# Kernel tuning notes

Hardware: AMD Instinct MI355X
Metric: run time of the kernel (lower is better)

Reference implementation:

```python
import jax, jax.numpy as jnp
import numpy as np
from jax import lax


def _conv_layer(x, K, k, stride, pad):
    """Faithful reimplementation of the custom Conv2d, including its two quirks:
    1) weight/input flatten-order mismatch: K.reshape(k*k*cin, cout) pairs flat
       index m (decoded as kh,kw,cin for K) against x flattened as (cin,kh,kw),
       so the effective conv weight is K.reshape(-1,cout).reshape(cin,k,k,cout).
    2) the python loop range(0, padd-k, stride) misses the last valid position
       whenever (padd-k) is divisible by stride, leaving last row/col zero.
    """
    B, cin, s_in, _ = x.shape
    cout = K.shape[-1]
    out_size = (s_in + 2 * pad - k) // stride + 1
    padd = s_in + 2 * pad
    n_loop = -(-(padd - k) // stride)  # = len(range(0, padd-k, stride))
    xp = jnp.pad(x, ((0, 0), (0, 0), (pad, pad), (pad, pad))) if pad > 0 else x
    # effective weight honoring the flatten-order mismatch: (cin, kh, kw, cout)
    W = K.reshape(-1, cout).reshape(cin, k, k, cout)
    y = lax.conv_general_dilated(
        xp, W, window_strides=(stride, stride), padding='VALID',
        dimension_numbers=('NCHW', 'IHWO', 'NCHW'))
    n = min(n_loop, out_size)
    out = jnp.zeros((B, cout, out_size, out_size), x.dtype)
    out = out.at[:, :, :n, :n].set(y[:, :, :n, :n])
    return out


def setup_inputs() -> dict:
    key = jax.random.key(0)
    ks = jax.random.split(key, 9)
    NUM_CLASSES = 10
    B = 8192

    def kinit(k_, shape):
        fan_in = shape[1] * int(np.prod(shape[2:]))  # torch fan_in for 4D
        bound = float(np.sqrt(6.0 / fan_in))
        return jax.random.uniform(k_, shape, jnp.float32, -bound, bound)

    x = jax.random.normal(ks[0], (B, 3, 28, 28), jnp.float32)
    K1 = kinit(ks[1], (5, 5, 3, 8))
    K2 = kinit(ks[2], (3, 3, 8, 16))
    K3 = kinit(ks[3], (3, 3, 16, 16))
    K4 = kinit(ks[4], (3, 3, 16, 16))
    K5 = kinit(ks[5], (3, 3, 16, 16))
    K6 = kinit(ks[6], (5, 5, 16, 32))
    fc_in = 6 * 6 * 32  # 1152
    bw = float(np.sqrt(1.0 / fc_in))
    Wfc = jax.random.uniform(ks[7], (NUM_CLASSES, fc_in), jnp.float32, -bw, bw)
    bfc = jax.random.uniform(ks[8], (NUM_CLASSES,), jnp.float32, -bw, bw)
    return {"x": x, "K1": K1, "K2": K2, "K3": K3, "K4": K4, "K5": K5,
            "K6": K6, "Wfc": Wfc, "bfc": bfc}


def reference(x, K1, K2, K3, K4, K5, K6, Wfc, bfc):
    h = jax.nn.relu(_conv_layer(x, K1, 5, 2, 1))   # (B,8,13,13)
    h = jax.nn.relu(_conv_layer(h, K2, 3, 1, 1))   # (B,16,13,13), last row/col zero
    h = jax.nn.relu(_conv_layer(h, K3, 3, 1, 1))
    h = jax.nn.relu(_conv_layer(h, K4, 3, 1, 1))
    h = jax.nn.relu(_conv_layer(h, K5, 3, 1, 1))
    h = _conv_layer(h, K6, 5, 2, 1)                # (B,32,6,6), last row/col zero
    flat = h.reshape(h.shape[0], -1)               # (B,1152)
    logits = flat @ Wfc.T + bfc
    return jax.nn.softmax(logits, axis=1)
```

## Files before the change

kernel.cpp:

```cpp
#include <hip/hip_runtime.h>
#include <math.h>

#define TPB 256

typedef __attribute__((ext_vector_type(8))) short short8;
typedef __attribute__((ext_vector_type(4))) float f32x4;
typedef unsigned short u16;

__device__ __forceinline__ f32x4 MFMA(short8 a, short8 b, f32x4 c) {
    return __builtin_amdgcn_mfma_f32_16x16x32_bf16(a, b, c, 0, 0, 0);
}
__device__ __forceinline__ u16 f2bf(float f) {
    unsigned int u = __builtin_bit_cast(unsigned int, f);
    u += 0x7FFFu + ((u >> 16) & 1u);
    return (u16)(u >> 16);
}
__device__ __forceinline__ float bf2f(u16 h) {
    unsigned int u = ((unsigned int)h) << 16;
    return __builtin_bit_cast(float, u);
}

extern "C" __global__ void prep_w(const float* __restrict__ K1, const float* __restrict__ K2,
                                  const float* __restrict__ K3, const float* __restrict__ K4,
                                  const float* __restrict__ K5, const float* __restrict__ K6,
                                  short8* __restrict__ W)
{
    const int slot = blockIdx.x * blockDim.x + threadIdx.x;
    if (slot >= 6144) return;
    const int lane = slot & 63;
    const int ent  = slot >> 6;
    const int o    = lane & 15;
    const int lhi  = lane >> 4;
    float w[8];
    int hl;
    if (ent < 6) {
        const int s = ent >> 1; hl = ent & 1;
        const int t = s * 4 + lhi;
#pragma unroll
        for (int j = 0; j < 8; j++)
            w[j] = (t < 9) ? K2[(j * 9 + t) * 16 + o] : 0.f;
    } else if (ent < 36) {
        const int e  = ent - 6;
        const float* Kg = (e < 10) ? K3 : (e < 20) ? K4 : K5;
        const int el = e % 10;
        const int s  = el >> 1; hl = el & 1;
        const int chalf = (lhi & 1) * 8;
        const int t = 2 * s + (lhi >> 1);
#pragma unroll
        for (int j = 0; j < 8; j++)
            w[j] = (t < 9) ? Kg[((chalf + j) * 9 + t) * 16 + o] : 0.f;
    } else if (ent < 88) {
        const int e = ent - 36;
        const int s = e >> 2; hl = (e >> 1) & 1;
        const int nh = e & 1;
        const int chalf = (lhi & 1) * 8;
        const int t  = 2 * s + (lhi >> 1);
        const int oo = nh * 16 + o;
#pragma unroll
        for (int j = 0; j < 8; j++)
            w[j] = (t < 25) ? K6[((chalf + j) * 25 + t) * 32 + oo] : 0.f;
    } else {
        const int e = ent - 88;
        const int s = e >> 1; hl = e & 1;
        const int g  = s * 4 + lhi;
        const int gc = g > 14 ? 14 : g;
        const int c  = (gc * 52) >> 8;
        const int kh = gc - 5 * c;
#pragma unroll
        for (int j = 0; j < 8; j++)
            w[j] = (g < 15 && o < 8 && j < 5) ? K1[(c * 25 + kh * 5 + j) * 8 + o] : 0.f;
    }
    short8 v;
#pragma unroll
    for (int j = 0; j < 8; j++) {
        const u16 h = f2bf(w[j]);
        v[j] = hl ? (short)f2bf(w[j] - bf2f(h)) : (short)h;
    }
    W[slot] = v;
}


__device__ __forceinline__ void conv8(const u16* __restrict__ s0,
                                      u16* __restrict__ d0,
                                      const short8* __restrict__ Wt,
                                      int wave, int lane, int rot)
{
    const int o   = lane & 15;
    const int lhi = lane >> 4;
    short8 Bhi[3], Blo[3];
#pragma unroll
    for (int s = 0; s < 3; s++) {
        Bhi[s] = Wt[(s * 2 + 0) * 64 + lane];
        Blo[s] = Wt[(s * 2 + 1) * 64 + lane];
    }
    const u16* sl = s0 + 3600;
    const int r0 = lane & 15;

    auto tile = [&](int m) {
        const int p  = m * 16 + r0;
        const int ip = (p * 683) >> 13;
        const int jp = p - 12 * ip;
        f32x4 acc = {0.f, 0.f, 0.f, 0.f};
#pragma unroll
        for (int s = 0; s < 3; s++) {
            const int t  = s * 4 + lhi;
            const int tt = t > 8 ? 8 : t;
            const int kh = (tt * 11) >> 5;
            const int kw = tt - 3 * kh;
            const int px = (ip + kh) * 15 + (jp + kw);
            const short8 Ahi = *(const short8*)(s0 + px * 8);
            const short8 Alo = *(const short8*)(sl + px * 8);
            acc = MFMA(Ahi, Bhi[s], acc);
            acc = MFMA(Alo, Bhi[s], acc);
            acc = MFMA(Ahi, Blo[s], acc);
        }
        const int p0 = m * 16 + lhi * 4;
#pragma unroll
        for (int r = 0; r < 4; r++) {
            const int pp = p0 + r;
            const int ii = (pp * 683) >> 13;
            const int jj = pp - 12 * ii;
            const float v = fmaxf(acc[r], 0.f);
            const u16 h = f2bf(v);
            const int px2 = (ii + 1) * 15 + (jj + 1);
            const int da  = (o >> 3) * 1800 + px2 * 8 + (o & 7);
            d0[da]        = h;
            d0[da + 3600] = f2bf(v - bf2f(h));
        }
    };
    const int m0 = (wave + rot) & 3;
    tile(m0);
    tile(m0 + 4);
    if (m0 == 0) tile(8);
}

__device__ __forceinline__ void conv16(const u16* __restrict__ s0,
                                       u16* __restrict__ d0,
                                       const short8* __restrict__ Wt,
                                       int wave, int lane, int rot)
{
    const int o    = lane & 15;
    const int lhi  = lane >> 4;
    const int hsel = lhi & 1;
    const int tsel = lhi >> 1;
    short8 Bhi[5], Blo[5];
#pragma unroll
    for (int s = 0; s < 5; s++) {
        Bhi[s] = Wt[(s * 2 + 0) * 64 + lane];
        Blo[s] = Wt[(s * 2 + 1) * 64 + lane];
    }
    const u16* sh = s0 + hsel * 1800;
    const u16* sl = sh + 3600;
    const int r0 = lane & 15;

    auto tile = [&](int m) {
        const int p  = m * 16 + r0;
        const int ip = (p * 683) >> 13;
        const int jp = p - 12 * ip;
        f32x4 acc = {0.f, 0.f, 0.f, 0.f};
#pragma unroll
        for (int s = 0; s < 5; s++) {
            const int t  = 2 * s + tsel;
            const int tt = t > 8 ? 8 : t;
            const int kh = (tt * 11) >> 5;
            const int kw = tt - 3 * kh;
            const int px = (ip + kh) * 15 + (jp + kw);
            const short8 Ahi = *(const short8*)(sh + px * 8);
            const short8 Alo = *(const short8*)(sl + px * 8);
            acc = MFMA(Ahi, Bhi[s], acc);
            acc = MFMA(Alo, Bhi[s], acc);
            acc = MFMA(Ahi, Blo[s], acc);
        }
        const int p0 = m * 16 + lhi * 4;
#pragma unroll
        for (int r = 0; r < 4; r++) {
            const int pp = p0 + r;
            const int ii = (pp * 683) >> 13;
            const int jj = pp - 12 * ii;
            const float v = fmaxf(acc[r], 0.f);
            const u16 h = f2bf(v);
            const int px2 = (ii + 1) * 15 + (jj + 1);
            const int da  = (o >> 3) * 1800 + px2 * 8 + (o & 7);
            d0[da]        = h;
            d0[da + 3600] = f2bf(v - bf2f(h));
        }
    };
    const int m0 = (wave + rot) & 3;
    tile(m0);
    tile(m0 + 4);
    if (m0 == 0) tile(8);
}

extern "C" __global__ void __launch_bounds__(TPB)
cnn_fused(const float* __restrict__ xg,
          const float* __restrict__ Wfc, const float* __restrict__ bfc,
          const short8* __restrict__ W, float* __restrict__ out)
{
    __shared__ __align__(16) unsigned char smem[40384];
    u16*   const Sh   = (u16*)smem;
    u16*   const Ah   = (u16*)(smem + 11520);
    u16*   const Bhp  = (u16*)(smem + 25920);
    float* const sF   = (float*)smem;
    float* const sLog = (float*)(smem + 40320);
    uint4* const z4   = (uint4*)smem;
    const uint4 Z = {0u, 0u, 0u, 0u};

    const int tid  = threadIdx.x;
    const int lane = tid & 63;
    const int wave = tid >> 6;
    const int img  = blockIdx.x;

    for (int i = tid; i < 2524; i += TPB) z4[i] = Z;
    __syncthreads();

    const float4* xi4 = (const float4*)(xg + (size_t)img * 2352);
    for (int i4 = tid; i4 < 588; i4 += TPB) {
        const float4 v = xi4[i4];
        const int c = i4 / 196;
        const int rem = i4 - c * 196;
        const int r = rem / 7;
        const int q = rem - r * 7;
        const int ad = c * 960 + (r + 1) * 32 + q * 4 + 1;
        const float vv[4] = {v.x, v.y, v.z, v.w};
#pragma unroll
        for (int e = 0; e < 4; e++) {
            const u16 h = f2bf(vv[e]);
            Sh[ad + e]        = h;
            Sh[ad + e + 2880] = f2bf(vv[e] - bf2f(h));
        }
    }
    __syncthreads();

    {
        const short8* Wt1 = W + 5632;
        const int o   = lane & 15;
        const int lhi = lane >> 4;
        short8 B1h[4], B1l[4];
#pragma unroll
        for (int s = 0; s < 4; s++) {
            B1h[s] = Wt1[(s * 2 + 0) * 64 + lane];
            B1l[s] = Wt1[(s * 2 + 1) * 64 + lane];
        }
        const u16* slo = Sh + 2880;
        for (int m = wave; m < 11; m += 4) {
            const int p  = m * 16 + o;
            const int pc = p > 168 ? 168 : p;
            const int i = (pc * 316) >> 12;
            const int j = pc - 13 * i;
            f32x4 acc = {0.f, 0.f, 0.f, 0.f};
#pragma unroll
            for (int s = 0; s < 4; s++) {
                const int g  = s * 4 + lhi;
                const int gc = g > 14 ? 14 : g;
                const int c  = (gc * 52) >> 8;
                const int kh = gc - 5 * c;
                const int ad = c * 960 + (2 * i + kh) * 32 + 2 * j;
                const short8 Ahi = *(const short8*)(Sh + ad);
                const short8 Alo = *(const short8*)(slo + ad);
                acc = MFMA(Ahi, B1h[s], acc);
                acc = MFMA(Alo, B1h[s], acc);
                acc = MFMA(Ahi, B1l[s], acc);
            }
#pragma unroll
            for (int r = 0; r < 4; r++) {
                const int pp = m * 16 + lhi * 4 + r;
                if (pp < 169 && o < 8) {
                    const int ii = (pp * 316) >> 12;
                    const int jj = pp - 13 * ii;
                    const float v = fmaxf(acc[r], 0.f);
                    const u16 h = f2bf(v);
                    const int da = ((ii + 1) * 15 + (jj + 1)) * 8 + o;
                    Bhp[da]        = h;
                    Bhp[da + 3600] = f2bf(v - bf2f(h));
                }
            }
        }
    }
    __syncthreads();

    for (int i = tid; i < 288; i += TPB) z4[i] = Z;

    conv8(Bhp, Ah, W, wave, lane, 0);
    __syncthreads();
    conv16(Ah, Bhp, W + 384, wave, lane, 1);
    __syncthreads();
    conv16(Bhp, Ah, W + 1024, wave, lane, 2);
    __syncthreads();
    conv16(Ah, Bhp, W + 1664, wave, lane, 3);
    __syncthreads();

    {
        const short8* Wt6 = W + 2304;
        const int mt   = wave >> 1;
        const int nh   = wave & 1;
        const int lhi  = lane >> 4;
        const int hsel = lhi & 1;
        const int tsel = lhi >> 1;
        const int o    = nh * 16 + (lane & 15);
        const int pr = mt * 16 + (lane & 15);
        const int pe = pr < 25 ? pr : 0;
        const int ia = (pe * 52) >> 8;
        const int ja = pe - 5 * ia;
        const u16* sh = Bhp + hsel * 1800;
        const u16* sl = sh + 3600;
        f32x4 acc = {0.f, 0.f, 0.f, 0.f};
#pragma unroll 4
        for (int s = 0; s < 13; s++) {
            const int t  = 2 * s + tsel;
            const int tt = t > 24 ? 24 : t;
            const int kh = (tt * 52) >> 8;
            const int kw = tt - 5 * kh;
            const int px = (2 * ia + kh) * 15 + (2 * ja + kw);
            const short8 Ahi = *(const short8*)(sh + px * 8);
            const short8 Alo = *(const short8*)(sl + px * 8);
            const short8 Bh2 = Wt6[((s * 2 + 0) * 2 + nh) * 64 + lane];
            const short8 Bl2 = Wt6[((s * 2 + 1) * 2 + nh) * 64 + lane];
            acc = MFMA(Ahi, Bh2, acc);
            acc = MFMA(Alo, Bh2, acc);
            acc = MFMA(Ahi, Bl2, acc);
        }
        const int p0 = mt * 16 + lhi * 4;
#pragma unroll
        for (int r = 0; r < 4; r++) {
            const int pp = p0 + r;
            if (pp < 25) {
                const int ii = (pp * 52) >> 8;
                const int jj = pp - 5 * ii;
                sF[o * 36 + ii * 6 + jj] = acc[r];
            }
        }
    }
    __syncthreads();

    if (tid < 160) {
        const int c = tid >> 4;
        const int l = tid & 15;
        const float4* fv = (const float4*)(sF + l * 72);
        const float4* wv = (const float4*)(Wfc + c * 1152 + l * 72);
        float p = 0.f;
#pragma unroll
        for (int m = 0; m < 18; m++) {
            const float4 a = fv[m];
            const float4 b = wv[m];
            p = fmaf(a.x, b.x, p);
            p = fmaf(a.y, b.y, p);
            p = fmaf(a.z, b.z, p);
            p = fmaf(a.w, b.w, p);
        }
        p += __shfl_down(p, 8, 16);
        p += __shfl_down(p, 4, 16);
        p += __shfl_down(p, 2, 16);
        p += __shfl_down(p, 1, 16);
        if (l == 0) sLog[c] = p + bfc[c];
    }
    __syncthreads();

    if (tid < 10) {
        float mx = sLog[0];
#pragma unroll
        for (int k = 1; k < 10; k++) mx = fmaxf(mx, sLog[k]);
        float s = 0.f;
#pragma unroll
        for (int k = 0; k < 10; k++) s += expf(sLog[k] - mx);
        out[(size_t)img * 10 + tid] = expf(sLog[tid] - mx) / s;
    }
}

extern "C" void kernel_launch(void* const* d_in, const int* in_sizes, int n_in,
                              void* d_out, int out_size, void* d_ws, size_t ws_size,
                              hipStream_t stream) {
    const float* x   = (const float*)d_in[0];
    const float* K1  = (const float*)d_in[1];
    const float* K2  = (const float*)d_in[2];
    const float* K3  = (const float*)d_in[3];
    const float* K4  = (const float*)d_in[4];
    const float* K5  = (const float*)d_in[5];
    const float* K6  = (const float*)d_in[6];
    const float* Wfc = (const float*)d_in[7];
    const float* bfc = (const float*)d_in[8];
    float* out = (float*)d_out;
    short8* W = (short8*)d_ws;

    prep_w<<<24, TPB, 0, stream>>>(K1, K2, K3, K4, K5, K6, W);

    const int B = in_sizes[0] / 2352;
    cnn_fused<<<B, TPB, 0, stream>>>(x, Wfc, bfc, W, out);
}
```

Baseline: 213.6 us.

## Use 512-thread blocks with eight waves and compact shared memory layout

Doubles the block to eight waves so each conv layer's nine M-tiles are spread across more waves, with each wave doing one tile instead of two. Shared memory is shrunk by aliasing the input staging buffer, the second ping-pong buffer and the FC scratch into one region, and the zeroing of padding borders is rearranged with extra barriers. The intent is more parallel MFMA work per image and higher occupancy from the smaller LDS footprint. In exchange the final conv6 stage runs on only half the waves, there are extra syncs, and register limits tighten under launch_bounds(512, 8).

After: 258.2 us. 1.21x slower.

```diff
diff --git a/kernel.cpp b/kernel.cpp
--- a/kernel.cpp
+++ b/kernel.cpp
@@ -1,7 +1,7 @@
 #include <hip/hip_runtime.h>
 #include <math.h>
 
-#define TPB 256
+#define TPB 512
 
 typedef __attribute__((ext_vector_type(8))) short short8;
 typedef __attribute__((ext_vector_type(4))) float f32x4;
@@ -128,9 +128,8 @@
             d0[da + 3600] = f2bf(v - bf2f(h));
         }
     };
-    const int m0 = (wave + rot) & 3;
+    const int m0 = (wave + rot) & 7;
     tile(m0);
-    tile(m0 + 4);
     if (m0 == 0) tile(8);
 }
 
@@ -185,23 +184,22 @@
             d0[da + 3600] = f2bf(v - bf2f(h));
         }
     };
-    const int m0 = (wave + rot) & 3;
+    const int m0 = (wave + rot) & 7;
     tile(m0);
-    tile(m0 + 4);
     if (m0 == 0) tile(8);
 }
 
-extern "C" __global__ void __launch_bounds__(TPB)
+extern "C" __global__ void __launch_bounds__(TPB, 8)
 cnn_fused(const float* __restrict__ xg,
           const float* __restrict__ Wfc, const float* __restrict__ bfc,
           const short8* __restrict__ W, float* __restrict__ out)
 {
-    __shared__ __align__(16) unsigned char smem[40384];
-    u16*   const Sh   = (u16*)smem;
-    u16*   const Ah   = (u16*)(smem + 11520);
-    u16*   const Bhp  = (u16*)(smem + 25920);
-    float* const sF   = (float*)smem;
-    float* const sLog = (float*)(smem + 40320);
+    __shared__ __align__(16) unsigned char smem[28864];
+    u16*   const Ah   = (u16*)smem;
+    u16*   const Bh   = (u16*)(smem + 14400);
+    u16*   const Sh   = (u16*)(smem + 14400);
+    float* const sF   = (float*)(smem + 14400);
+    float* const sLog = (float*)(smem + 28800);
     uint4* const z4   = (uint4*)smem;
     const uint4 Z = {0u, 0u, 0u, 0u};
 
@@ -210,7 +208,7 @@
     const int wave = tid >> 6;
     const int img  = blockIdx.x;
 
-    for (int i = tid; i < 2524; i += TPB) z4[i] = Z;
+    for (int i = tid; i < 1804; i += TPB) z4[i] = Z;
     __syncthreads();
 
     const float4* xi4 = (const float4*)(xg + (size_t)img * 2352);
@@ -242,7 +240,7 @@
             B1l[s] = Wt1[(s * 2 + 1) * 64 + lane];
         }
         const u16* slo = Sh + 2880;
-        for (int m = wave; m < 11; m += 4) {
+        for (int m = wave; m < 11; m += 8) {
             const int p  = m * 16 + o;
             const int pc = p > 168 ? 168 : p;
             const int i = (pc * 316) >> 12;
@@ -270,26 +268,30 @@
                     const float v = fmaxf(acc[r], 0.f);
                     const u16 h = f2bf(v);
                     const int da = ((ii + 1) * 15 + (jj + 1)) * 8 + o;
-                    Bhp[da]        = h;
-                    Bhp[da + 3600] = f2bf(v - bf2f(h));
+                    Ah[da]        = h;
+                    Ah[da + 3600] = f2bf(v - bf2f(h));
                 }
             }
         }
     }
     __syncthreads();
 
-    for (int i = tid; i < 288; i += TPB) z4[i] = Z;
-
-    conv8(Bhp, Ah, W, wave, lane, 0);
-    __syncthreads();
-    conv16(Ah, Bhp, W + 384, wave, lane, 1);
-    __syncthreads();
-    conv16(Bhp, Ah, W + 1024, wave, lane, 2);
-    __syncthreads();
-    conv16(Ah, Bhp, W + 1664, wave, lane, 3);
-    __syncthreads();
-
-    {
+    for (int i = tid; i < 900; i += TPB) z4[900 + i] = Z;
+    __syncthreads();
+
+    conv8(Ah, Bh, W, wave, lane, 0);
+    __syncthreads();
+    conv16(Bh, Ah, W + 384, wave, lane, 1);
+    __syncthreads();
+    conv16(Ah, Bh, W + 1024, wave, lane, 2);
+    __syncthreads();
+    conv16(Bh, Ah, W + 1664, wave, lane, 3);
+    __syncthreads();
+
+    for (int i = tid; i < 288; i += TPB) z4[900 + i] = Z;
+    __syncthreads();
+
+    if (wave < 4) {
         const short8* Wt6 = W + 2304;
         const int mt   = wave >> 1;
         const int nh   = wave & 1;
@@ -301,7 +303,7 @@
         const int pe = pr < 25 ? pr : 0;
         const int ia = (pe * 52) >> 8;
         const int ja = pe - 5 * ia;
-        const u16* sh = Bhp + hsel * 1800;
+        const u16* sh = Ah + hsel * 1800;
         const u16* sl = sh + 3600;
         f32x4 acc = {0.f, 0.f, 0.f, 0.f};
 #pragma unroll 4
@@ -381,7 +383,7 @@
     float* out = (float*)d_out;
     short8* W = (short8*)d_ws;
 
-    prep_w<<<24, TPB, 0, stream>>>(K1, K2, K3, K4, K5, K6, W);
+    prep_w<<<24, 256, 0, stream>>>(K1, K2, K3, K4, K5, K6, W);
 
     const int B = in_sizes[0] / 2352;
     cnn_fused<<<B, TPB, 0, stream>>>(x, Wfc, bfc, W, out);
```
